# Optimization experiments

Hardware: AMD Instinct MI355X
Metric: run time of the kernel (lower is better)

## Reference

```python
import jax, jax.numpy as jnp
import numpy as np

N_NODES = 50000
N_EDGES = 800000
H = 128
D = 128
N_LAYERS = 4
N_GRAPHS = 128
NODE_VOCAB = 32
EDGE_VOCAB = 8
BN_EPS = 1e-5


def _bn(h, g, b):
    # BatchNorm1d, training-mode statistics (biased variance), as in the torch module
    m = h.mean(axis=0)
    v = ((h - m) ** 2).mean(axis=0)
    return (h - m) * jax.lax.rsqrt(v + BN_EPS) * g + b


def _gine(x, src, dst, e, eps_l):
    # GINEConv: message = ReLU(x_src + edge_attr), sum-aggregate at dst
    msg = jax.nn.relu(x[src] + e)                      # [E, H]
    aggr = jax.ops.segment_sum(msg, dst, num_segments=N_NODES)
    return (1.0 + eps_l) * x + aggr


def _forward(x_ids, edge_index, batch, edge_attr,
             node_emb, edge_emb, eps,
             init_W1, init_b1, init_g1, init_be1, init_W2, init_b2, init_g2, init_be2,
             mp_W1, mp_g1, mp_be1, mp_W2, mp_g2, mp_be2,
             l1_W1, l1_g1, l1_b1, l1_W2, l1_g2, l1_b2,
             l2_W1, l2_g1, l2_b1, l2_W2, l2_g2, l2_b2,
             fin_W):
    src, dst = edge_index[0], edge_index[1]
    x = node_emb[x_ids]                                # [N, H]
    e = edge_emb[edge_attr]                            # [E, H]
    # initialization conv (Linear layers WITH bias)
    h = _gine(x, src, dst, e, eps[0])
    h = jax.nn.relu(_bn(h @ init_W1 + init_b1, init_g1, init_be1))
    x = jax.nn.relu(_bn(h @ init_W2 + init_b2, init_g2, init_be2))
    # message-passing layers (Linear layers WITHOUT bias)
    for i in range(N_LAYERS):
        h = _gine(x, src, dst, e, eps[1 + i])
        h = jax.nn.relu(_bn(h @ mp_W1[i], mp_g1[i], mp_be1[i]))
        x = jax.nn.relu(_bn(h @ mp_W2[i], mp_g2[i], mp_be2[i]))
    # readout: global_add_pool
    g = jax.ops.segment_sum(x, batch, num_segments=N_GRAPHS)   # [G, H]
    # lin1 (outer F.relu is idempotent; dropout = identity in eval)
    h = jax.nn.relu(_bn(g @ l1_W1, l1_g1, l1_b1))
    h = jax.nn.relu(_bn(h @ l1_W2, l1_g2, l1_b2))
    # lin2
    h = jax.nn.relu(_bn(h @ l2_W1, l2_g1, l2_b1))
    h = jax.nn.relu(_bn(h @ l2_W2, l2_g2, l2_b2))
    return h @ fin_W                                   # [G, 1]


def setup_inputs() -> dict:
    key = jax.random.key(0)
    ks = jax.random.split(key, 20)
    s = 1.0 / np.sqrt(H)
    rn = lambda k, shp, sc: jax.random.normal(k, shp, dtype=jnp.float32) * sc
    return {
        "x_ids": jax.random.randint(ks[0], (N_NODES,), 0, NODE_VOCAB),
        "edge_index": jax.random.randint(ks[1], (2, N_EDGES), 0, N_NODES),
        "batch": jnp.sort(jax.random.randint(ks[2], (N_NODES,), 0, N_GRAPHS)),
        "edge_attr": jax.random.randint(ks[14], (N_EDGES,), 0, EDGE_VOCAB),
        "node_emb": rn(ks[3], (NODE_VOCAB, H), 0.05),
        "edge_emb": rn(ks[4], (EDGE_VOCAB, H), 0.05),
        "eps": jnp.zeros((N_LAYERS + 1,), jnp.float32),
        "init_W1": rn(ks[5], (H, D), s), "init_b1": jnp.zeros((D,)),
        "init_g1": jnp.ones((D,)), "init_be1": jnp.zeros((D,)),
        "init_W2": rn(ks[6], (D, H), s), "init_b2": jnp.zeros((H,)),
        "init_g2": jnp.ones((H,)), "init_be2": jnp.zeros((H,)),
        "mp_W1": rn(ks[7], (N_LAYERS, H, D), s),
        "mp_g1": jnp.ones((N_LAYERS, D)), "mp_be1": jnp.zeros((N_LAYERS, D)),
        "mp_W2": rn(ks[8], (N_LAYERS, D, H), s),
        "mp_g2": jnp.ones((N_LAYERS, H)), "mp_be2": jnp.zeros((N_LAYERS, H)),
        "l1_W1": rn(ks[9], (H, D), s), "l1_g1": jnp.ones((D,)), "l1_b1": jnp.zeros((D,)),
        "l1_W2": rn(ks[10], (D, D), s), "l1_g2": jnp.ones((D,)), "l1_b2": jnp.zeros((D,)),
        "l2_W1": rn(ks[11], (D, D), s), "l2_g1": jnp.ones((D,)), "l2_b1": jnp.zeros((D,)),
        "l2_W2": rn(ks[12], (D, H), s), "l2_g2": jnp.ones((H,)), "l2_b2": jnp.zeros((H,)),
        "fin_W": rn(ks[13], (H, 1), s),
    }


def reference(x_ids, edge_index, batch, edge_attr,
              node_emb, edge_emb, eps,
              init_W1, init_b1, init_g1, init_be1, init_W2, init_b2, init_g2, init_be2,
              mp_W1, mp_g1, mp_be1, mp_W2, mp_g2, mp_be2,
              l1_W1, l1_g1, l1_b1, l1_W2, l1_g2, l1_b2,
              l2_W1, l2_g1, l2_b1, l2_W2, l2_g2, l2_b2,
              fin_W):
    return _forward(x_ids, edge_index, batch, edge_attr,
                    node_emb, edge_emb, eps,
                    init_W1, init_b1, init_g1, init_be1, init_W2, init_b2, init_g2, init_be2,
                    mp_W1, mp_g1, mp_be1, mp_W2, mp_g2, mp_be2,
                    l1_W1, l1_g1, l1_b1, l1_W2, l1_g2, l1_b2,
                    l2_W1, l2_g1, l2_b1, l2_W2, l2_g2, l2_b2,
                    fin_W)
```

## Files before the change

kernel.cpp:

```cpp
#include <hip/hip_runtime.h>

#define NN 50000
#define NE 800000
#define NG 128
#define HD 128
#define NL 4
#define BN_EPS 1e-5f
#define REP 32
#define WP 136
#define NB 392
#define EPB 4096

typedef __attribute__((ext_vector_type(8))) short bf16x8;
typedef __attribute__((ext_vector_type(4))) float f32x4;

__device__ __forceinline__ unsigned short f2bf(float f) {
    unsigned u = __float_as_uint(f);
    u += 0x7FFFu + ((u >> 16) & 1u);
    return (unsigned short)(u >> 16);
}
__device__ __forceinline__ float bfval(unsigned short h) { return __uint_as_float((unsigned)h << 16); }
__device__ __forceinline__ float bflo(unsigned u) { return __uint_as_float(u << 16); }
__device__ __forceinline__ float bfhi(unsigned u) { return __uint_as_float(u & 0xFFFF0000u); }

__device__ __forceinline__ void split2(float a, float b, unsigned& hi, unsigned& lo) {
    unsigned ua = __float_as_uint(a), ub = __float_as_uint(b);
    hi = (ua >> 16) | (ub & 0xFFFF0000u);
    float ra = a - __uint_as_float(ua & 0xFFFF0000u);
    float rb = b - __uint_as_float(ub & 0xFFFF0000u);
    lo = (unsigned)f2bf(ra) | ((unsigned)f2bf(rb) << 16);
}
__device__ __forceinline__ unsigned pack2(float a, float b) {
    return (unsigned)f2bf(a) | ((unsigned)f2bf(b) << 16);
}

__device__ __forceinline__ void bn_pre(const float* SQbase,
                                       const float* gam, const float* bet,
                                       float inv_cnt, int t, float* scs, float* shs) {
    if (gam == nullptr) { scs[t] = 1.f; shs[t] = 0.f; return; }
    float s = 0.f, q = 0.f;
#pragma unroll
    for (int r = 0; r < REP; r++) {
        s += SQbase[r * 256 + t];
        q += SQbase[r * 256 + 128 + t];
    }
    float m = s * inv_cnt;
    float var = fmaxf(fmaf(q, inv_cnt, -m * m), 0.f);
    float inv = rsqrtf(var + BN_EPS);
    float sc = gam[t] * inv;
    scs[t] = sc;
    shs[t] = fmaf(-m, sc, bet[t]);
}

__global__ __launch_bounds__(256) void setup_kernel(const int* __restrict__ ids,
                                                    const float* __restrict__ emb,
                                                    unsigned short* __restrict__ Yb,
                                                    const float* __restrict__ iw1,
                                                    const float* __restrict__ iw2,
                                                    const float* __restrict__ mw1,
                                                    const float* __restrict__ mw2,
                                                    const float* __restrict__ hw1,
                                                    const float* __restrict__ hw2,
                                                    const float* __restrict__ hw3,
                                                    const float* __restrict__ hw4,
                                                    unsigned short* __restrict__ Wh,
                                                    unsigned short* __restrict__ Wl,
                                                    const int* __restrict__ dst,
                                                    int* __restrict__ deg) {
    int b = blockIdx.x, t = threadIdx.x;
    if (b < 3125) {
        int i = b * 256 + t;
        if (i < NN * 16) {
            int node = i >> 4, g = i & 15;
            int id = ids[node];
            const float* p = emb + (size_t)id * HD + 8 * g;
            float4 a = *(const float4*)p;
            float4 bb = *(const float4*)(p + 4);
            uint4 o;
            o.x = pack2(a.x, a.y); o.y = pack2(a.z, a.w);
            o.z = pack2(bb.x, bb.y); o.w = pack2(bb.z, bb.w);
            *(uint4*)(Yb + (size_t)node * HD + 8 * g) = o;
        }
    } else if (b < 4021) {
        int i = (b - 3125) * 256 + t;
        if (i < 229376) {
            int seg = i >> 14, loc = i & 16383;
            float v;
            if (seg == 0)       v = iw1[loc];
            else if (seg == 1)  v = iw2[loc];
            else if (seg < 6)   v = mw1[(seg - 2) * 16384 + loc];
            else if (seg < 10)  v = mw2[(seg - 6) * 16384 + loc];
            else if (seg == 10) v = hw1[loc];
            else if (seg == 11) v = hw2[loc];
            else if (seg == 12) v = hw3[loc];
            else                v = hw4[loc];
            int k = loc >> 7, n = loc & 127;
            unsigned short h = f2bf(v);
            float r = v - bfval(h);
            Wh[seg * 16384 + n * 128 + k] = h;
            Wl[seg * 16384 + n * 128 + k] = f2bf(r);
        }
    } else {
        int e = (b - 4021) * 256 + t;
        if (e < NE) atomicAdd(&deg[dst[e]], 1);
    }
}

__global__ __launch_bounds__(256) void ybn_kernel(const float* __restrict__ X,
                                                  const float* __restrict__ SQin,
                                                  const float* __restrict__ gam,
                                                  const float* __restrict__ bet,
                                                  unsigned short* __restrict__ Yb) {
    __shared__ float scs[HD], shs[HD];
    int t = threadIdx.x;
    if (t < HD) bn_pre(SQin, gam, bet, 1.f / NN, t, scs, shs);
    __syncthreads();
    int c8 = (t & 15) * 8;
    float4 s0 = *(const float4*)&scs[c8], s1 = *(const float4*)&scs[c8 + 4];
    float4 h0 = *(const float4*)&shs[c8], h1 = *(const float4*)&shs[c8 + 4];
#pragma unroll
    for (int ch = 0; ch < 4; ch++) {
        int row = blockIdx.x * 64 + ch * 16 + (t >> 4);
        if (row < NN) {
            const float* p = X + (size_t)row * HD + c8;
            float4 v0 = *(const float4*)p;
            float4 v1 = *(const float4*)(p + 4);
            float f0 = fmaxf(fmaf(v0.x, s0.x, h0.x), 0.f), f1 = fmaxf(fmaf(v0.y, s0.y, h0.y), 0.f);
            float f2 = fmaxf(fmaf(v0.z, s0.z, h0.z), 0.f), f3 = fmaxf(fmaf(v0.w, s0.w, h0.w), 0.f);
            float f4 = fmaxf(fmaf(v1.x, s1.x, h1.x), 0.f), f5 = fmaxf(fmaf(v1.y, s1.y, h1.y), 0.f);
            float f6 = fmaxf(fmaf(v1.z, s1.z, h1.z), 0.f), f7 = fmaxf(fmaf(v1.w, s1.w, h1.w), 0.f);
            uint4 o;
            o.x = pack2(f0, f1); o.y = pack2(f2, f3);
            o.z = pack2(f4, f5); o.w = pack2(f6, f7);
            *(uint4*)(Yb + (size_t)row * HD + c8) = o;
        }
    }
}

__global__ __launch_bounds__(1024) void scan1_kernel(const int* __restrict__ deg,
                                                     int* __restrict__ rowptr,
                                                     int* __restrict__ blockSum) {
    __shared__ int s[1024];
    int b = blockIdx.x, t = threadIdx.x;
    int i = b * 1024 + t;
    int v = (i < NN) ? deg[i] : 0;
    s[t] = v;
    __syncthreads();
    for (int off = 1; off < 1024; off <<= 1) {
        int u = (t >= off) ? s[t - off] : 0;
        __syncthreads();
        s[t] += u;
        __syncthreads();
    }
    if (i < NN) rowptr[i] = s[t] - v;
    if (t == 1023) blockSum[b] = s[1023];
}

__global__ __launch_bounds__(64) void scan2_kernel(const int* __restrict__ blockSum,
                                                   int* __restrict__ blockOff,
                                                   int* __restrict__ rowptr, int nblocks) {
    int t = threadIdx.x;
    int orig = (t < nblocks) ? blockSum[t] : 0;
    int v = orig;
    for (int off = 1; off < 64; off <<= 1) {
        int u = __shfl_up(v, off, 64);
        if (t >= off) v += u;
    }
    if (t < nblocks) blockOff[t] = v - orig;
    if (t == nblocks - 1) rowptr[NN] = v;
}

__global__ __launch_bounds__(1024) void scan3_kernel(int* __restrict__ rowptr,
                                                     int* __restrict__ cursor,
                                                     const int* __restrict__ blockOff,
                                                     int* __restrict__ bucketCursor) {
    int b = blockIdx.x, t = threadIdx.x;
    int i = b * 1024 + t;
    if (i < NN) {
        int r = rowptr[i] + blockOff[b];
        rowptr[i] = r;
        cursor[i] = r;
        if ((i & 127) == 0) bucketCursor[i >> 7] = r;
    }
}

__global__ __launch_bounds__(256) void bin_kernel(const int* __restrict__ src,
                                                  const int* __restrict__ dst,
                                                  const int* __restrict__ attr,
                                                  int* __restrict__ bucketCursor,
                                                  uint2* __restrict__ ebuf) {
    __shared__ int cnt[512];
    __shared__ int sc[512], sc2[512];
    __shared__ int base[512];
    __shared__ int garr[NB];
    __shared__ int wof[NB];
    __shared__ uint2 stage[EPB];
    int t = threadIdx.x;
    int e0 = blockIdx.x * EPB;
    for (int i = t; i < 512; i += 256) cnt[i] = 0;
    __syncthreads();
    int myb[16]; unsigned myv[16]; int myd[16];
#pragma unroll
    for (int j = 0; j < 16; j++) {
        int e = e0 + t + j * 256;
        if (e < NE) {
            int d = dst[e];
            myd[j] = d;
            myv[j] = (unsigned)src[e] | ((unsigned)attr[e] << 16);
            myb[j] = d >> 7;
            atomicAdd(&cnt[myb[j]], 1);
        } else myb[j] = -1;
    }
    __syncthreads();
    for (int k = t; k < 512; k += 256) sc[k] = cnt[k];
    __syncthreads();
    int* sp = sc; int* dp = sc2;
    for (int off = 1; off < 512; off <<= 1) {
        for (int k = t; k < 512; k += 256) dp[k] = sp[k] + (k >= off ? sp[k - off] : 0);
        __syncthreads();
        int* tmp = sp; sp = dp; dp = tmp;
    }
    for (int k = t; k < 512; k += 256) base[k] = sp[k] - cnt[k];
    int total = sp[511];
    __syncthreads();
    for (int b = t; b < NB; b += 256) {
        wof[b] = 0;
        if (cnt[b] > 0) garr[b] = atomicAdd(&bucketCursor[b], cnt[b]);
    }
    __syncthreads();
#pragma unroll
    for (int j = 0; j < 16; j++) {
        if (myb[j] >= 0) {
            int slot = base[myb[j]] + atomicAdd(&wof[myb[j]], 1);
            stage[slot] = make_uint2(myv[j], (unsigned)myd[j]);
        }
    }
    __syncthreads();
    for (int i = t; i < total; i += 256) {
        uint2 u = stage[i];
        int b = (int)(u.y >> 7);
        ebuf[garr[b] + (i - base[b])] = u;
    }
}

__global__ __launch_bounds__(256) void place_kernel(const uint2* __restrict__ ebuf,
                                                    const int* __restrict__ rowptr,
                                                    int* __restrict__ cursor,
                                                    unsigned* __restrict__ csr) {
    int b = blockIdx.x;
    int n0 = b * 128;
    int n1 = n0 + 128; if (n1 > NN) n1 = NN;
    int es = rowptr[n0], ee = rowptr[n1];
    for (int i = es + threadIdx.x; i < ee; i += 256) {
        uint2 u = ebuf[i];
        int pos = atomicAdd(&cursor[u.y], 1);
        csr[pos] = u.x;
    }
}

__device__ __forceinline__ void gine_acc(const unsigned short* __restrict__ Yb,
                                         const float* __restrict__ elds,
                                         unsigned p, int cq, float mask, float* a) {
    uint4 q = *(const uint4*)(Yb + (size_t)(p & 0xFFFFu) * HD + 8 * cq);
    const float* ep = elds + (p >> 16) * HD + 8 * cq;
    float4 e0 = *(const float4*)ep;
    float4 e1 = *(const float4*)(ep + 4);
    a[0] += mask * fmaxf(bflo(q.x) + e0.x, 0.f);
    a[1] += mask * fmaxf(bfhi(q.x) + e0.y, 0.f);
    a[2] += mask * fmaxf(bflo(q.y) + e0.z, 0.f);
    a[3] += mask * fmaxf(bfhi(q.y) + e0.w, 0.f);
    a[4] += mask * fmaxf(bflo(q.z) + e1.x, 0.f);
    a[5] += mask * fmaxf(bfhi(q.z) + e1.y, 0.f);
    a[6] += mask * fmaxf(bflo(q.w) + e1.z, 0.f);
    a[7] += mask * fmaxf(bfhi(q.w) + e1.w, 0.f);
}

__global__ __launch_bounds__(256) void conv_kernel(const unsigned short* __restrict__ Yb,
                                                   const int* __restrict__ rowptr,
                                                   const unsigned* __restrict__ csr,
                                                   const float* __restrict__ edge_emb,
                                                   const float* __restrict__ eps, int layer,
                                                   unsigned short* __restrict__ Ah,
                                                   unsigned short* __restrict__ Al) {
    __shared__ float elds[8 * HD];
    int t = threadIdx.x;
    ((float4*)elds)[t] = ((const float4*)edge_emb)[t];
    __syncthreads();
    int wave = t >> 6, lane = t & 63;
    int node = blockIdx.x * 4 + wave;
    if (node >= NN) return;
    int sub = lane >> 4, cq = lane & 15;
    int lo = rowptr[node], hi = rowptr[node + 1];
    float a[8];
#pragma unroll
    for (int i = 0; i < 8; i++) a[i] = 0.f;
    for (int base = lo; base < hi; base += 64) {
        unsigned pl = 0;
        int cnt = hi - base; if (cnt > 64) cnt = 64;
        if (base + lane < hi) pl = csr[base + lane];
        int j = 0;
        for (; j + 16 <= cnt; j += 16) {
            unsigned pa = __shfl(pl, j + sub, 64);
            unsigned pb = __shfl(pl, j + 4 + sub, 64);
            unsigned pc = __shfl(pl, j + 8 + sub, 64);
            unsigned pd = __shfl(pl, j + 12 + sub, 64);
            gine_acc(Yb, elds, pa, cq, 1.f, a);
            gine_acc(Yb, elds, pb, cq, 1.f, a);
            gine_acc(Yb, elds, pc, cq, 1.f, a);
            gine_acc(Yb, elds, pd, cq, 1.f, a);
        }
        for (; j + 8 <= cnt; j += 8) {
            unsigned pa = __shfl(pl, j + sub, 64);
            unsigned pb = __shfl(pl, j + 4 + sub, 64);
            gine_acc(Yb, elds, pa, cq, 1.f, a);
            gine_acc(Yb, elds, pb, cq, 1.f, a);
        }
        for (; j < cnt; j += 4) {
            int je = j + sub;
            bool val = (je < cnt);
            unsigned p = __shfl(pl, val ? je : j, 64);
            gine_acc(Yb, elds, p, cq, val ? 1.f : 0.f, a);
        }
    }
#pragma unroll
    for (int i = 0; i < 8; i++) {
        a[i] += __shfl_xor(a[i], 16, 64);
        a[i] += __shfl_xor(a[i], 32, 64);
    }
    if (sub == 0) {
        float g = 1.f + eps[layer];
        uint4 q = *(const uint4*)(Yb + (size_t)node * HD + 8 * cq);
        float o0 = fmaf(g, bflo(q.x), a[0]), o1 = fmaf(g, bfhi(q.x), a[1]);
        float o2 = fmaf(g, bflo(q.y), a[2]), o3 = fmaf(g, bfhi(q.y), a[3]);
        float o4 = fmaf(g, bflo(q.z), a[4]), o5 = fmaf(g, bfhi(q.z), a[5]);
        float o6 = fmaf(g, bflo(q.w), a[6]), o7 = fmaf(g, bfhi(q.w), a[7]);
        uint4 H, L;
        split2(o0, o1, H.x, L.x);
        split2(o2, o3, H.y, L.y);
        split2(o4, o5, H.z, L.z);
        split2(o6, o7, H.w, L.w);
        *(uint4*)(Ah + (size_t)node * HD + 8 * cq) = H;
        *(uint4*)(Al + (size_t)node * HD + 8 * cq) = L;
    }
}

__global__ __launch_bounds__(512) void mm_mfma_pre(const unsigned short* __restrict__ Ah,
                                                   const unsigned short* __restrict__ Al,
                                                   const unsigned short* __restrict__ Wh,
                                                   const unsigned short* __restrict__ Wl,
                                                   const float* __restrict__ bias,
                                                   float* __restrict__ out,
                                                   float* __restrict__ SQout) {
    __shared__ unsigned short WhS[128 * WP];
    __shared__ unsigned short WlS[128 * WP];
    int t = threadIdx.x;
    int rowblk = blockIdx.x;
#pragma unroll
    for (int i = 0; i < 4; i++) {
        int idx = t + i * 512;
        int col = idx >> 4, kk = (idx & 15) * 8;
        *(uint4*)(WhS + col * WP + kk) = *(const uint4*)(Wh + (size_t)col * HD + kk);
        *(uint4*)(WlS + col * WP + kk) = *(const uint4*)(Wl + (size_t)col * HD + kk);
    }
    __syncthreads();
    int w = t >> 6, lane = t & 63;
    int quad = lane >> 4, nl = lane & 15;
    int row0 = rowblk * 128 + w * 16;
    int rA0 = row0 + nl;
    bool ok0 = rA0 < NN;
    f32x4 acc[8];
#pragma unroll
    for (int i = 0; i < 8; i++) acc[i] = (f32x4){0.f, 0.f, 0.f, 0.f};
#pragma unroll
    for (int kc = 0; kc < 4; kc++) {
        int k0 = kc * 32 + quad * 8;
        bf16x8 a0h = ok0 ? *(const bf16x8*)(Ah + (size_t)rA0 * HD + k0) : (bf16x8)0;
        bf16x8 a0l = ok0 ? *(const bf16x8*)(Al + (size_t)rA0 * HD + k0) : (bf16x8)0;
#pragma unroll
        for (int c = 0; c < 8; c++) {
            int wof = (c * 16 + nl) * WP + k0;
            bf16x8 bh = *(const bf16x8*)(WhS + wof);
            bf16x8 bl = *(const bf16x8*)(WlS + wof);
            acc[c] = __builtin_amdgcn_mfma_f32_16x16x32_bf16(a0h, bh, acc[c], 0, 0, 0);
            acc[c] = __builtin_amdgcn_mfma_f32_16x16x32_bf16(a0l, bh, acc[c], 0, 0, 0);
            acc[c] = __builtin_amdgcn_mfma_f32_16x16x32_bf16(a0h, bl, acc[c], 0, 0, 0);
        }
    }
    int rep = (blockIdx.x & (REP - 1)) * 256;
    int baserow = row0 + quad * 4;
#pragma unroll
    for (int c = 0; c < 8; c++) {
        int col = c * 16 + nl;
        float bv = bias ? bias[col] : 0.f;
        f32x4 v = acc[c];
        float s = 0.f, qq = 0.f;
#pragma unroll
        for (int r = 0; r < 4; r++) {
            int grow = baserow + r;
            float val = v[r] + bv;
            if (grow < NN) {
                out[(size_t)grow * HD + col] = val;
                s += val;
                qq += val * val;
            }
        }
        s += __shfl_xor(s, 16, 64);  s += __shfl_xor(s, 32, 64);
        qq += __shfl_xor(qq, 16, 64); qq += __shfl_xor(qq, 32, 64);
        if (quad == 0) {
            atomicAdd(&SQout[rep + col], s);
            atomicAdd(&SQout[rep + 128 + col], qq);
        }
    }
}

__global__ __launch_bounds__(512) void mm_mfma_act(const float* __restrict__ A,
                                                   const unsigned short* __restrict__ Wh,
                                                   const unsigned short* __restrict__ Wl,
                                                   const float* __restrict__ bias,
                                                   const float* __restrict__ SQin,
                                                   const float* __restrict__ gam,
                                                   const float* __restrict__ bet,
                                                   float* __restrict__ out,
                                                   float* __restrict__ SQout) {
    __shared__ unsigned short WhS[128 * WP];
    __shared__ unsigned short WlS[128 * WP];
    __shared__ float scs[HD], shs[HD];
    int t = threadIdx.x;
    int rowblk = blockIdx.x;
    if (t < HD) bn_pre(SQin, gam, bet, 1.f / NN, t, scs, shs);
#pragma unroll
    for (int i = 0; i < 4; i++) {
        int idx = t + i * 512;
        int col = idx >> 4, kk = (idx & 15) * 8;
        *(uint4*)(WhS + col * WP + kk) = *(const uint4*)(Wh + (size_t)col * HD + kk);
        *(uint4*)(WlS + col * WP + kk) = *(const uint4*)(Wl + (size_t)col * HD + kk);
    }
    __syncthreads();
    int w = t >> 6, lane = t & 63;
    int quad = lane >> 4, nl = lane & 15;
    int row0 = rowblk * 128 + w * 16;
    int rA0 = row0 + nl;
    bool ok0 = rA0 < NN;
    f32x4 acc[8];
#pragma unroll
    for (int i = 0; i < 8; i++) acc[i] = (f32x4){0.f, 0.f, 0.f, 0.f};
#pragma unroll
    for (int kc = 0; kc < 4; kc++) {
        int k0 = kc * 32 + quad * 8;
        float4 s0 = *(const float4*)&scs[k0], s1 = *(const float4*)&scs[k0 + 4];
        float4 t0 = *(const float4*)&shs[k0], t1 = *(const float4*)&shs[k0 + 4];
        bf16x8 a0h, a0l;
        {
            float4 v0 = ok0 ? *(const float4*)(A + (size_t)rA0 * HD + k0) : make_float4(0, 0, 0, 0);
            float4 v1 = ok0 ? *(const float4*)(A + (size_t)rA0 * HD + k0 + 4) : make_float4(0, 0, 0, 0);
            float f0 = fmaxf(fmaf(v0.x, s0.x, t0.x), 0.f), f1 = fmaxf(fmaf(v0.y, s0.y, t0.y), 0.f);
            float f2 = fmaxf(fmaf(v0.z, s0.z, t0.z), 0.f), f3 = fmaxf(fmaf(v0.w, s0.w, t0.w), 0.f);
            float f4 = fmaxf(fmaf(v1.x, s1.x, t1.x), 0.f), f5 = fmaxf(fmaf(v1.y, s1.y, t1.y), 0.f);
            float f6 = fmaxf(fmaf(v1.z, s1.z, t1.z), 0.f), f7 = fmaxf(fmaf(v1.w, s1.w, t1.w), 0.f);
            if (!ok0) { f0 = f1 = f2 = f3 = f4 = f5 = f6 = f7 = 0.f; }
            unsigned h0, h1, h2, h3, l0, l1, l2, l3;
            split2(f0, f1, h0, l0); split2(f2, f3, h1, l1);
            split2(f4, f5, h2, l2); split2(f6, f7, h3, l3);
            a0h = __builtin_bit_cast(bf16x8, make_uint4(h0, h1, h2, h3));
            a0l = __builtin_bit_cast(bf16x8, make_uint4(l0, l1, l2, l3));
        }
#pragma unroll
        for (int c = 0; c < 8; c++) {
            int wof = (c * 16 + nl) * WP + k0;
            bf16x8 bh = *(const bf16x8*)(WhS + wof);
            bf16x8 bl = *(const bf16x8*)(WlS + wof);
            acc[c] = __builtin_amdgcn_mfma_f32_16x16x32_bf16(a0h, bh, acc[c], 0, 0, 0);
            acc[c] = __builtin_amdgcn_mfma_f32_16x16x32_bf16(a0l, bh, acc[c], 0, 0, 0);
            acc[c] = __builtin_amdgcn_mfma_f32_16x16x32_bf16(a0h, bl, acc[c], 0, 0, 0);
        }
    }
    int rep = (blockIdx.x & (REP - 1)) * 256;
    int baserow = row0 + quad * 4;
#pragma unroll
    for (int c = 0; c < 8; c++) {
        int col = c * 16 + nl;
        float bv = bias ? bias[col] : 0.f;
        f32x4 v = acc[c];
        float s = 0.f, qq = 0.f;
#pragma unroll
        for (int r = 0; r < 4; r++) {
            int grow = baserow + r;
            float val = v[r] + bv;
            if (grow < NN) {
                out[(size_t)grow * HD + col] = val;
                s += val;
                qq += val * val;
            }
        }
        s += __shfl_xor(s, 16, 64);  s += __shfl_xor(s, 32, 64);
        qq += __shfl_xor(qq, 16, 64); qq += __shfl_xor(qq, 32, 64);
        if (quad == 0) {
            atomicAdd(&SQout[rep + col], s);
            atomicAdd(&SQout[rep + 128 + col], qq);
        }
    }
}

__global__ __launch_bounds__(256) void readout_kernel(const float* __restrict__ x,
                                                      const int* __restrict__ batch,
                                                      const float* __restrict__ SQin,
                                                      const float* __restrict__ gam,
                                                      const float* __restrict__ bet,
                                                      float* __restrict__ gout) {
    __shared__ int bat[256];
    __shared__ float scs[HD], shs[HD];
    int t = threadIdx.x;
    int rq = t >> 5, cq = t & 31;
    int r0 = blockIdx.x * 256;
    int i = r0 + t;
    bat[t] = (i < NN) ? batch[i] : -1;
    if (t < HD) bn_pre(SQin, gam, bet, 1.f / NN, t, scs, shs);
    __syncthreads();
    float4 s4 = *(const float4*)&scs[4 * cq];
    float4 h4 = *(const float4*)&shs[4 * cq];
    float4 acc = make_float4(0.f, 0.f, 0.f, 0.f);
    int gcur = -1;
    for (int j = rq; j < 256; j += 8) {
        int r = r0 + j;
        if (r >= NN) break;
        int g = bat[j];
        if (g != gcur) {
            if (gcur >= 0) {
                atomicAdd(&gout[(size_t)gcur * HD + 4 * cq + 0], acc.x);
                atomicAdd(&gout[(size_t)gcur * HD + 4 * cq + 1], acc.y);
                atomicAdd(&gout[(size_t)gcur * HD + 4 * cq + 2], acc.z);
                atomicAdd(&gout[(size_t)gcur * HD + 4 * cq + 3], acc.w);
            }
            acc = make_float4(0.f, 0.f, 0.f, 0.f);
            gcur = g;
        }
        float4 v = *(const float4*)(x + (size_t)r * HD + 4 * cq);
        acc.x += fmaxf(fmaf(v.x, s4.x, h4.x), 0.f);
        acc.y += fmaxf(fmaf(v.y, s4.y, h4.y), 0.f);
        acc.z += fmaxf(fmaf(v.z, s4.z, h4.z), 0.f);
        acc.w += fmaxf(fmaf(v.w, s4.w, h4.w), 0.f);
    }
    if (gcur >= 0) {
        atomicAdd(&gout[(size_t)gcur * HD + 4 * cq + 0], acc.x);
        atomicAdd(&gout[(size_t)gcur * HD + 4 * cq + 1], acc.y);
        atomicAdd(&gout[(size_t)gcur * HD + 4 * cq + 2], acc.z);
        atomicAdd(&gout[(size_t)gcur * HD + 4 * cq + 3], acc.w);
    }
}

__device__ __forceinline__ void head_stage(const unsigned short* __restrict__ Whg,
                                           const unsigned short* __restrict__ Wlg,
                                           const float* __restrict__ gam,
                                           const float* __restrict__ bet,
                                           float* A_lds,
                                           unsigned short* WhS, unsigned short* WlS,
                                           float* colS, float* colQ,
                                           float* scs, float* shs) {
    const int AP = 132;
    int t = threadIdx.x;
#pragma unroll
    for (int i = 0; i < 2; i++) {
        int idx = t + i * 1024;
        int col = idx >> 4, kk = (idx & 15) * 8;
        *(uint4*)(WhS + col * WP + kk) = *(const uint4*)(Whg + (size_t)col * HD + kk);
        *(uint4*)(WlS + col * WP + kk) = *(const uint4*)(Wlg + (size_t)col * HD + kk);
    }
    __syncthreads();
    int w = t >> 6, lane = t & 63;
    int quad = lane >> 4, nl = lane & 15;
    int row0 = (w >> 2) * 32, col0 = (w & 3) * 32;
    f32x4 acc[4];
#pragma unroll
    for (int i = 0; i < 4; i++) acc[i] = (f32x4){0.f, 0.f, 0.f, 0.f};
#pragma unroll
    for (int kc = 0; kc < 4; kc++) {
        int k0 = kc * 32 + quad * 8;
        float4 s0 = *(const float4*)&scs[k0], s1 = *(const float4*)&scs[k0 + 4];
        float4 t0 = *(const float4*)&shs[k0], t1 = *(const float4*)&shs[k0 + 4];
        bf16x8 a0h, a0l, a1h, a1l;
        {
            const float* ap = &A_lds[(row0 + nl) * AP + k0];
            float4 v0 = *(const float4*)ap;
            float4 v1 = *(const float4*)(ap + 4);
            float f0 = fmaxf(fmaf(v0.x, s0.x, t0.x), 0.f), f1 = fmaxf(fmaf(v0.y, s0.y, t0.y), 0.f);
            float f2 = fmaxf(fmaf(v0.z, s0.z, t0.z), 0.f), f3 = fmaxf(fmaf(v0.w, s0.w, t0.w), 0.f);
            float f4 = fmaxf(fmaf(v1.x, s1.x, t1.x), 0.f), f5 = fmaxf(fmaf(v1.y, s1.y, t1.y), 0.f);
            float f6 = fmaxf(fmaf(v1.z, s1.z, t1.z), 0.f), f7 = fmaxf(fmaf(v1.w, s1.w, t1.w), 0.f);
            unsigned h0, h1, h2, h3, l0, l1, l2, l3;
            split2(f0, f1, h0, l0); split2(f2, f3, h1, l1);
            split2(f4, f5, h2, l2); split2(f6, f7, h3, l3);
            a0h = __builtin_bit_cast(bf16x8, make_uint4(h0, h1, h2, h3));
            a0l = __builtin_bit_cast(bf16x8, make_uint4(l0, l1, l2, l3));
        }
        {
            const float* ap = &A_lds[(row0 + 16 + nl) * AP + k0];
            float4 v0 = *(const float4*)ap;
            float4 v1 = *(const float4*)(ap + 4);
            float f0 = fmaxf(fmaf(v0.x, s0.x, t0.x), 0.f), f1 = fmaxf(fmaf(v0.y, s0.y, t0.y), 0.f);
            float f2 = fmaxf(fmaf(v0.z, s0.z, t0.z), 0.f), f3 = fmaxf(fmaf(v0.w, s0.w, t0.w), 0.f);
            float f4 = fmaxf(fmaf(v1.x, s1.x, t1.x), 0.f), f5 = fmaxf(fmaf(v1.y, s1.y, t1.y), 0.f);
            float f6 = fmaxf(fmaf(v1.z, s1.z, t1.z), 0.f), f7 = fmaxf(fmaf(v1.w, s1.w, t1.w), 0.f);
            unsigned h0, h1, h2, h3, l0, l1, l2, l3;
            split2(f0, f1, h0, l0); split2(f2, f3, h1, l1);
            split2(f4, f5, h2, l2); split2(f6, f7, h3, l3);
            a1h = __builtin_bit_cast(bf16x8, make_uint4(h0, h1, h2, h3));
            a1l = __builtin_bit_cast(bf16x8, make_uint4(l0, l1, l2, l3));
        }
#pragma unroll
        for (int cc = 0; cc < 2; cc++) {
            int wof = (col0 + cc * 16 + nl) * WP + k0;
            bf16x8 bh = *(const bf16x8*)(WhS + wof);
            bf16x8 bl = *(const bf16x8*)(WlS + wof);
            acc[cc] = __builtin_amdgcn_mfma_f32_16x16x32_bf16(a0h, bh, acc[cc], 0, 0, 0);
            acc[cc] = __builtin_amdgcn_mfma_f32_16x16x32_bf16(a0l, bh, acc[cc], 0, 0, 0);
            acc[cc] = __builtin_amdgcn_mfma_f32_16x16x32_bf16(a0h, bl, acc[cc], 0, 0, 0);
            acc[2 + cc] = __builtin_amdgcn_mfma_f32_16x16x32_bf16(a1h, bh, acc[2 + cc], 0, 0, 0);
            acc[2 + cc] = __builtin_amdgcn_mfma_f32_16x16x32_bf16(a1l, bh, acc[2 + cc], 0, 0, 0);
            acc[2 + cc] = __builtin_amdgcn_mfma_f32_16x16x32_bf16(a1h, bl, acc[2 + cc], 0, 0, 0);
        }
    }
    __syncthreads();
#pragma unroll
    for (int h = 0; h < 2; h++) {
        int baserow = row0 + h * 16 + quad * 4;
#pragma unroll
        for (int cc = 0; cc < 2; cc++) {
            int col = col0 + cc * 16 + nl;
            f32x4 v = acc[h * 2 + cc];
            float ss = 0.f, qq = 0.f;
#pragma unroll
            for (int r = 0; r < 4; r++) {
                float val = v[r];
                A_lds[(baserow + r) * AP + col] = val;
                ss += val;
                qq += val * val;
            }
            ss += __shfl_xor(ss, 16, 64);  ss += __shfl_xor(ss, 32, 64);
            qq += __shfl_xor(qq, 16, 64);  qq += __shfl_xor(qq, 32, 64);
            if (quad == 0) {
                atomicAdd(&colS[col], ss);
                atomicAdd(&colQ[col], qq);
            }
        }
    }
    __syncthreads();
    if (t < HD) {
        float m = colS[t] * (1.f / NG);
        float var = fmaxf(fmaf(colQ[t], 1.f / NG, -m * m), 0.f);
        float inv = rsqrtf(var + BN_EPS);
        float sc = gam[t] * inv;
        scs[t] = sc;
        shs[t] = fmaf(-m, sc, bet[t]);
        colS[t] = 0.f;
        colQ[t] = 0.f;
    }
    __syncthreads();
}

__global__ __launch_bounds__(1024) void head_fused(const float* __restrict__ Gp,
                                                   const unsigned short* __restrict__ Whd,
                                                   const unsigned short* __restrict__ Wld,
                                                   const float* __restrict__ g0,
                                                   const float* __restrict__ b0,
                                                   const float* __restrict__ g1,
                                                   const float* __restrict__ b1,
                                                   const float* __restrict__ g2,
                                                   const float* __restrict__ b2,
                                                   const float* __restrict__ g3,
                                                   const float* __restrict__ b3,
                                                   const float* __restrict__ finW,
                                                   float* __restrict__ out) {
    const int AP = 132;
    __shared__ float A_lds[128 * AP];
    __shared__ unsigned short WhS[128 * WP];
    __shared__ unsigned short WlS[128 * WP];
    __shared__ float colS[HD], colQ[HD], scs[HD], shs[HD];
    int t = threadIdx.x;
    if (t < HD) { colS[t] = 0.f; colQ[t] = 0.f; scs[t] = 1.f; shs[t] = 0.f; }
#pragma unroll
    for (int i = 0; i < 4; i++) {
        int idx = t + i * 1024;
        int r = idx >> 5, cq = (idx & 31) * 4;
        *(float4*)&A_lds[r * AP + cq] = *(const float4*)(Gp + (size_t)r * HD + cq);
    }
    head_stage(Whd + 0 * 16384, Wld + 0 * 16384, g0, b0, A_lds, WhS, WlS, colS, colQ, scs, shs);
    head_stage(Whd + 1 * 16384, Wld + 1 * 16384, g1, b1, A_lds, WhS, WlS, colS, colQ, scs, shs);
    head_stage(Whd + 2 * 16384, Wld + 2 * 16384, g2, b2, A_lds, WhS, WlS, colS, colQ, scs, shs);
    head_stage(Whd + 3 * 16384, Wld + 3 * 16384, g3, b3, A_lds, WhS, WlS, colS, colQ, scs, shs);
    int r = t >> 3, g = t & 7;
    float ssum = 0.f;
#pragma unroll
    for (int j = 0; j < 16; j++) {
        int c = g * 16 + j;
        float v = fmaxf(fmaf(A_lds[r * AP + c], scs[c], shs[c]), 0.f);
        ssum += v * finW[c];
    }
    ssum += __shfl_xor(ssum, 1, 64);
    ssum += __shfl_xor(ssum, 2, 64);
    ssum += __shfl_xor(ssum, 4, 64);
    if (g == 0) out[r] = ssum;
}

extern "C" void kernel_launch(void* const* d_in, const int* in_sizes, int n_in,
                              void* d_out, int out_size, void* d_ws, size_t ws_size,
                              hipStream_t stream) {
    const int* x_ids = (const int*)d_in[0];
    const int* edge_index = (const int*)d_in[1];
    const int* batch = (const int*)d_in[2];
    const int* edge_attr = (const int*)d_in[3];
    const float* node_emb = (const float*)d_in[4];
    const float* edge_emb = (const float*)d_in[5];
    const float* eps = (const float*)d_in[6];
    const float* init_W1 = (const float*)d_in[7];
    const float* init_b1 = (const float*)d_in[8];
    const float* init_g1 = (const float*)d_in[9];
    const float* init_be1 = (const float*)d_in[10];
    const float* init_W2 = (const float*)d_in[11];
    const float* init_b2 = (const float*)d_in[12];
    const float* init_g2 = (const float*)d_in[13];
    const float* init_be2 = (const float*)d_in[14];
    const float* mp_W1 = (const float*)d_in[15];
    const float* mp_g1 = (const float*)d_in[16];
    const float* mp_be1 = (const float*)d_in[17];
    const float* mp_W2 = (const float*)d_in[18];
    const float* mp_g2 = (const float*)d_in[19];
    const float* mp_be2 = (const float*)d_in[20];
    const float* l1_W1 = (const float*)d_in[21];
    const float* l1_g1 = (const float*)d_in[22];
    const float* l1_b1 = (const float*)d_in[23];
    const float* l1_W2 = (const float*)d_in[24];
    const float* l1_g2 = (const float*)d_in[25];
    const float* l1_b2 = (const float*)d_in[26];
    const float* l2_W1 = (const float*)d_in[27];
    const float* l2_g1 = (const float*)d_in[28];
    const float* l2_b1 = (const float*)d_in[29];
    const float* l2_W2 = (const float*)d_in[30];
    const float* l2_g2 = (const float*)d_in[31];
    const float* l2_b2 = (const float*)d_in[32];
    const float* fin_W = (const float*)d_in[33];

    const int* e_src = edge_index;
    const int* e_dst = edge_index + NE;

    const size_t STG = (size_t)REP * 256;
    float* ws = (float*)d_ws;
    float* X = ws;
    float* Bbuf = X + (size_t)NN * HD;
    unsigned short* Yb = (unsigned short*)Bbuf;
    unsigned short* Ah = (unsigned short*)(Bbuf + (size_t)NN * HD);
    unsigned short* Al = Ah + (size_t)NN * HD;
    float* SQ = (float*)(Al + (size_t)NN * HD);
    float* Gp = SQ + 14 * STG;
    int* deg = (int*)(Gp + NG * HD);
    float* Hp = (float*)(deg + 50048);
    float* Hp2 = Hp + NG * HD;
    int* rowptr = (int*)(Hp2 + NG * HD);
    int* cursor = rowptr + 50048;
    int* blockSum = cursor + 50048;
    int* blockOff = blockSum + 64;
    int* bucketCursor = blockOff + 64;
    unsigned* csr = (unsigned*)(bucketCursor + NB);
    unsigned short* Wh = (unsigned short*)(csr + NE);
    unsigned short* Wl = Wh + 229376;
    uint2* ebuf = (uint2*)(Wl + 229376);
    (void)Hp; (void)Hp2;

    const size_t zero_bytes = (14 * STG + NG * HD) * sizeof(float) + 50048 * sizeof(int);
    hipMemsetAsync(SQ, 0, zero_bytes, stream);

    const int SCAN_BLOCKS = (NN + 1023) / 1024;
    setup_kernel<<<7146, 256, 0, stream>>>(x_ids, node_emb, Yb, init_W1, init_W2, mp_W1,
                                           mp_W2, l1_W1, l1_W2, l2_W1, l2_W2,
                                           Wh, Wl, e_dst, deg);
    scan1_kernel<<<SCAN_BLOCKS, 1024, 0, stream>>>(deg, rowptr, blockSum);
    scan2_kernel<<<1, 64, 0, stream>>>(blockSum, blockOff, rowptr, SCAN_BLOCKS);
    scan3_kernel<<<SCAN_BLOCKS, 1024, 0, stream>>>(rowptr, cursor, blockOff, bucketCursor);
    bin_kernel<<<(NE + EPB - 1) / EPB, 256, 0, stream>>>(e_src, e_dst, edge_attr,
                                                         bucketCursor, ebuf);
    place_kernel<<<(NN + 127) / 128, 256, 0, stream>>>(ebuf, rowptr, cursor, csr);

    const int mfma_grid = (NN + 127) / 128;
    const int ybn_grid = (NN + 63) / 64;
    for (int i = 0; i <= NL; i++) {
        const unsigned short* Wh1 = Wh + (size_t)(i == 0 ? 0 : 2 + (i - 1)) * 16384;
        const unsigned short* Wl1 = Wl + (size_t)(i == 0 ? 0 : 2 + (i - 1)) * 16384;
        const unsigned short* Wh2 = Wh + (size_t)(i == 0 ? 1 : 6 + (i - 1)) * 16384;
        const unsigned short* Wl2 = Wl + (size_t)(i == 0 ? 1 : 6 + (i - 1)) * 16384;
        const float* b1 = (i == 0) ? init_b1 : nullptr;
        const float* b2 = (i == 0) ? init_b2 : nullptr;
        const float* g1 = (i == 0) ? init_g1 : mp_g1 + (size_t)(i - 1) * HD;
        const float* be1 = (i == 0) ? init_be1 : mp_be1 + (size_t)(i - 1) * HD;
        const float* gp = (i == 1) ? init_g2 : mp_g2 + (size_t)(i - 2) * HD;
        const float* bp = (i == 1) ? init_be2 : mp_be2 + (size_t)(i - 2) * HD;
        float* Sprev = SQ + (size_t)(2 * i - 1) * STG;
        float* S1 = SQ + (size_t)(2 * i) * STG;
        float* S2 = SQ + (size_t)(2 * i + 1) * STG;

        if (i > 0) ybn_kernel<<<ybn_grid, 256, 0, stream>>>(X, Sprev, gp, bp, Yb);
        conv_kernel<<<(NN + 3) / 4, 256, 0, stream>>>(Yb, rowptr, csr, edge_emb, eps, i, Ah, Al);
        mm_mfma_pre<<<mfma_grid, 512, 0, stream>>>(Ah, Al, Wh1, Wl1, b1, Bbuf, S1);
        mm_mfma_act<<<mfma_grid, 512, 0, stream>>>(Bbuf, Wh2, Wl2, b2, S1, g1, be1, X, S2);
    }

    float* S9 = SQ + 9 * STG;
    readout_kernel<<<(NN + 255) / 256, 256, 0, stream>>>(
        X, batch, S9, mp_g2 + 3 * HD, mp_be2 + 3 * HD, Gp);

    head_fused<<<1, 1024, 0, stream>>>(Gp, Wh + (size_t)10 * 16384, Wl + (size_t)10 * 16384,
                                       l1_g1, l1_b1, l1_g2, l1_b2,
                                       l2_g1, l2_b1, l2_g2, l2_b2,
                                       fin_W, (float*)d_out);
}
```

Baseline: 686.0 us.

## Fold scan2 into scan3, specialize full-tile epilogues, prefetch head weights

Removes the single-wave scan2 launch by having every scan3 block recompute the 64-entry block-offset prefix in its first wave, saving one kernel launch in the setup chain. The matmul epilogues get a branch-free path for full 128-row tiles, dropping per-row bounds checks. The head kernel inlines its four stages and prefetches the next stage's weights into registers while the current stage computes. The cost is redundant prefix work in each scan3 block and some code growth from the duplicated epilogue.

```diff
diff --git a/kernel.cpp b/kernel.cpp
--- a/kernel.cpp
+++ b/kernel.cpp
@@ -156,32 +156,32 @@
     if (t == 1023) blockSum[b] = s[1023];
 }
 
-__global__ __launch_bounds__(64) void scan2_kernel(const int* __restrict__ blockSum,
-                                                   int* __restrict__ blockOff,
-                                                   int* __restrict__ rowptr, int nblocks) {
-    int t = threadIdx.x;
-    int orig = (t < nblocks) ? blockSum[t] : 0;
-    int v = orig;
-    for (int off = 1; off < 64; off <<= 1) {
-        int u = __shfl_up(v, off, 64);
-        if (t >= off) v += u;
-    }
-    if (t < nblocks) blockOff[t] = v - orig;
-    if (t == nblocks - 1) rowptr[NN] = v;
-}
-
 __global__ __launch_bounds__(1024) void scan3_kernel(int* __restrict__ rowptr,
                                                      int* __restrict__ cursor,
-                                                     const int* __restrict__ blockOff,
-                                                     int* __restrict__ bucketCursor) {
+                                                     const int* __restrict__ blockSum,
+                                                     int* __restrict__ bucketCursor,
+                                                     int nblocks) {
+    __shared__ int sOff, sTot;
     int b = blockIdx.x, t = threadIdx.x;
+    if (t < 64) {
+        int orig = (t < nblocks) ? blockSum[t] : 0;
+        int v = orig;
+        for (int off = 1; off < 64; off <<= 1) {
+            int u = __shfl_up(v, off, 64);
+            if (t >= off) v += u;
+        }
+        if (t == b) sOff = v - orig;
+        if (t == nblocks - 1) sTot = v;
+    }
+    __syncthreads();
     int i = b * 1024 + t;
     if (i < NN) {
-        int r = rowptr[i] + blockOff[b];
+        int r = rowptr[i] + sOff;
         rowptr[i] = r;
         cursor[i] = r;
         if ((i & 127) == 0) bucketCursor[i >> 7] = r;
     }
+    if (b == nblocks - 1 && t == 0) rowptr[NN] = sTot;
 }
 
 __global__ __launch_bounds__(256) void bin_kernel(const int* __restrict__ src,
@@ -388,27 +388,50 @@
     }
     int rep = (blockIdx.x & (REP - 1)) * 256;
     int baserow = row0 + quad * 4;
-#pragma unroll
-    for (int c = 0; c < 8; c++) {
-        int col = c * 16 + nl;
-        float bv = bias ? bias[col] : 0.f;
-        f32x4 v = acc[c];
-        float s = 0.f, qq = 0.f;
-#pragma unroll
-        for (int r = 0; r < 4; r++) {
-            int grow = baserow + r;
-            float val = v[r] + bv;
-            if (grow < NN) {
-                out[(size_t)grow * HD + col] = val;
+    if (rowblk * 128 + 128 <= NN) {
+#pragma unroll
+        for (int c = 0; c < 8; c++) {
+            int col = c * 16 + nl;
+            float bv = bias ? bias[col] : 0.f;
+            f32x4 v = acc[c];
+            float s = 0.f, qq = 0.f;
+#pragma unroll
+            for (int r = 0; r < 4; r++) {
+                float val = v[r] + bv;
+                out[(size_t)(baserow + r) * HD + col] = val;
                 s += val;
                 qq += val * val;
             }
-        }
-        s += __shfl_xor(s, 16, 64);  s += __shfl_xor(s, 32, 64);
-        qq += __shfl_xor(qq, 16, 64); qq += __shfl_xor(qq, 32, 64);
-        if (quad == 0) {
-            atomicAdd(&SQout[rep + col], s);
-            atomicAdd(&SQout[rep + 128 + col], qq);
+            s += __shfl_xor(s, 16, 64);  s += __shfl_xor(s, 32, 64);
+            qq += __shfl_xor(qq, 16, 64); qq += __shfl_xor(qq, 32, 64);
+            if (quad == 0) {
+                atomicAdd(&SQout[rep + col], s);
+                atomicAdd(&SQout[rep + 128 + col], qq);
+            }
+        }
+    } else {
+#pragma unroll
+        for (int c = 0; c < 8; c++) {
+            int col = c * 16 + nl;
+            float bv = bias ? bias[col] : 0.f;
+            f32x4 v = acc[c];
+            float s = 0.f, qq = 0.f;
+#pragma unroll
+            for (int r = 0; r < 4; r++) {
+                int grow = baserow + r;
+                float val = v[r] + bv;
+                if (grow < NN) {
+                    out[(size_t)grow * HD + col] = val;
+                    s += val;
+                    qq += val * val;
+                }
+            }
+            s += __shfl_xor(s, 16, 64);  s += __shfl_xor(s, 32, 64);
+            qq += __shfl_xor(qq, 16, 64); qq += __shfl_xor(qq, 32, 64);
+            if (quad == 0) {
+                atomicAdd(&SQout[rep + col], s);
+                atomicAdd(&SQout[rep + 128 + col], qq);
+            }
         }
     }
 }
@@ -476,27 +499,50 @@
     }
     int rep = (blockIdx.x & (REP - 1)) * 256;
     int baserow = row0 + quad * 4;
-#pragma unroll
-    for (int c = 0; c < 8; c++) {
-        int col = c * 16 + nl;
-        float bv = bias ? bias[col] : 0.f;
-        f32x4 v = acc[c];
-        float s = 0.f, qq = 0.f;
-#pragma unroll
-        for (int r = 0; r < 4; r++) {
-            int grow = baserow + r;
-            float val = v[r] + bv;
-            if (grow < NN) {
-                out[(size_t)grow * HD + col] = val;
+    if (rowblk * 128 + 128 <= NN) {
+#pragma unroll
+        for (int c = 0; c < 8; c++) {
+            int col = c * 16 + nl;
+            float bv = bias ? bias[col] : 0.f;
+            f32x4 v = acc[c];
+            float s = 0.f, qq = 0.f;
+#pragma unroll
+            for (int r = 0; r < 4; r++) {
+                float val = v[r] + bv;
+                out[(size_t)(baserow + r) * HD + col] = val;
                 s += val;
                 qq += val * val;
             }
-        }
-        s += __shfl_xor(s, 16, 64);  s += __shfl_xor(s, 32, 64);
-        qq += __shfl_xor(qq, 16, 64); qq += __shfl_xor(qq, 32, 64);
-        if (quad == 0) {
-            atomicAdd(&SQout[rep + col], s);
-            atomicAdd(&SQout[rep + 128 + col], qq);
+            s += __shfl_xor(s, 16, 64);  s += __shfl_xor(s, 32, 64);
+            qq += __shfl_xor(qq, 16, 64); qq += __shfl_xor(qq, 32, 64);
+            if (quad == 0) {
+                atomicAdd(&SQout[rep + col], s);
+                atomicAdd(&SQout[rep + 128 + col], qq);
+            }
+        }
+    } else {
+#pragma unroll
+        for (int c = 0; c < 8; c++) {
+            int col = c * 16 + nl;
+            float bv = bias ? bias[col] : 0.f;
+            f32x4 v = acc[c];
+            float s = 0.f, qq = 0.f;
+#pragma unroll
+            for (int r = 0; r < 4; r++) {
+                int grow = baserow + r;
+                float val = v[r] + bv;
+                if (grow < NN) {
+                    out[(size_t)grow * HD + col] = val;
+                    s += val;
+                    qq += val * val;
+                }
+            }
+            s += __shfl_xor(s, 16, 64);  s += __shfl_xor(s, 32, 64);
+            qq += __shfl_xor(qq, 16, 64); qq += __shfl_xor(qq, 32, 64);
+            if (quad == 0) {
+                atomicAdd(&SQout[rep + col], s);
+                atomicAdd(&SQout[rep + 128 + col], qq);
+            }
         }
     }
 }
@@ -546,115 +592,6 @@
         atomicAdd(&gout[(size_t)gcur * HD + 4 * cq + 2], acc.z);
         atomicAdd(&gout[(size_t)gcur * HD + 4 * cq + 3], acc.w);
     }
-}
-
-__device__ __forceinline__ void head_stage(const unsigned short* __restrict__ Whg,
-                                           const unsigned short* __restrict__ Wlg,
-                                           const float* __restrict__ gam,
-                                           const float* __restrict__ bet,
-                                           float* A_lds,
-                                           unsigned short* WhS, unsigned short* WlS,
-                                           float* colS, float* colQ,
-                                           float* scs, float* shs) {
-    const int AP = 132;
-    int t = threadIdx.x;
-#pragma unroll
-    for (int i = 0; i < 2; i++) {
-        int idx = t + i * 1024;
-        int col = idx >> 4, kk = (idx & 15) * 8;
-        *(uint4*)(WhS + col * WP + kk) = *(const uint4*)(Whg + (size_t)col * HD + kk);
-        *(uint4*)(WlS + col * WP + kk) = *(const uint4*)(Wlg + (size_t)col * HD + kk);
-    }
-    __syncthreads();
-    int w = t >> 6, lane = t & 63;
-    int quad = lane >> 4, nl = lane & 15;
-    int row0 = (w >> 2) * 32, col0 = (w & 3) * 32;
-    f32x4 acc[4];
-#pragma unroll
-    for (int i = 0; i < 4; i++) acc[i] = (f32x4){0.f, 0.f, 0.f, 0.f};
-#pragma unroll
-    for (int kc = 0; kc < 4; kc++) {
-        int k0 = kc * 32 + quad * 8;
-        float4 s0 = *(const float4*)&scs[k0], s1 = *(const float4*)&scs[k0 + 4];
-        float4 t0 = *(const float4*)&shs[k0], t1 = *(const float4*)&shs[k0 + 4];
-        bf16x8 a0h, a0l, a1h, a1l;
-        {
-            const float* ap = &A_lds[(row0 + nl) * AP + k0];
-            float4 v0 = *(const float4*)ap;
-            float4 v1 = *(const float4*)(ap + 4);
-            float f0 = fmaxf(fmaf(v0.x, s0.x, t0.x), 0.f), f1 = fmaxf(fmaf(v0.y, s0.y, t0.y), 0.f);
-            float f2 = fmaxf(fmaf(v0.z, s0.z, t0.z), 0.f), f3 = fmaxf(fmaf(v0.w, s0.w, t0.w), 0.f);
-            float f4 = fmaxf(fmaf(v1.x, s1.x, t1.x), 0.f), f5 = fmaxf(fmaf(v1.y, s1.y, t1.y), 0.f);
-            float f6 = fmaxf(fmaf(v1.z, s1.z, t1.z), 0.f), f7 = fmaxf(fmaf(v1.w, s1.w, t1.w), 0.f);
-            unsigned h0, h1, h2, h3, l0, l1, l2, l3;
-            split2(f0, f1, h0, l0); split2(f2, f3, h1, l1);
-            split2(f4, f5, h2, l2); split2(f6, f7, h3, l3);
-            a0h = __builtin_bit_cast(bf16x8, make_uint4(h0, h1, h2, h3));
-            a0l = __builtin_bit_cast(bf16x8, make_uint4(l0, l1, l2, l3));
-        }
-        {
-            const float* ap = &A_lds[(row0 + 16 + nl) * AP + k0];
-            float4 v0 = *(const float4*)ap;
-            float4 v1 = *(const float4*)(ap + 4);
-            float f0 = fmaxf(fmaf(v0.x, s0.x, t0.x), 0.f), f1 = fmaxf(fmaf(v0.y, s0.y, t0.y), 0.f);
-            float f2 = fmaxf(fmaf(v0.z, s0.z, t0.z), 0.f), f3 = fmaxf(fmaf(v0.w, s0.w, t0.w), 0.f);
-            float f4 = fmaxf(fmaf(v1.x, s1.x, t1.x), 0.f), f5 = fmaxf(fmaf(v1.y, s1.y, t1.y), 0.f);
-            float f6 = fmaxf(fmaf(v1.z, s1.z, t1.z), 0.f), f7 = fmaxf(fmaf(v1.w, s1.w, t1.w), 0.f);
-            unsigned h0, h1, h2, h3, l0, l1, l2, l3;
-            split2(f0, f1, h0, l0); split2(f2, f3, h1, l1);
-            split2(f4, f5, h2, l2); split2(f6, f7, h3, l3);
-            a1h = __builtin_bit_cast(bf16x8, make_uint4(h0, h1, h2, h3));
-            a1l = __builtin_bit_cast(bf16x8, make_uint4(l0, l1, l2, l3));
-        }
-#pragma unroll
-        for (int cc = 0; cc < 2; cc++) {
-            int wof = (col0 + cc * 16 + nl) * WP + k0;
-            bf16x8 bh = *(const bf16x8*)(WhS + wof);
-            bf16x8 bl = *(const bf16x8*)(WlS + wof);
-            acc[cc] = __builtin_amdgcn_mfma_f32_16x16x32_bf16(a0h, bh, acc[cc], 0, 0, 0);
-            acc[cc] = __builtin_amdgcn_mfma_f32_16x16x32_bf16(a0l, bh, acc[cc], 0, 0, 0);
-            acc[cc] = __builtin_amdgcn_mfma_f32_16x16x32_bf16(a0h, bl, acc[cc], 0, 0, 0);
-            acc[2 + cc] = __builtin_amdgcn_mfma_f32_16x16x32_bf16(a1h, bh, acc[2 + cc], 0, 0, 0);
-            acc[2 + cc] = __builtin_amdgcn_mfma_f32_16x16x32_bf16(a1l, bh, acc[2 + cc], 0, 0, 0);
-            acc[2 + cc] = __builtin_amdgcn_mfma_f32_16x16x32_bf16(a1h, bl, acc[2 + cc], 0, 0, 0);
-        }
-    }
-    __syncthreads();
-#pragma unroll
-    for (int h = 0; h < 2; h++) {
-        int baserow = row0 + h * 16 + quad * 4;
-#pragma unroll
-        for (int cc = 0; cc < 2; cc++) {
-            int col = col0 + cc * 16 + nl;
-            f32x4 v = acc[h * 2 + cc];
-            float ss = 0.f, qq = 0.f;
-#pragma unroll
-            for (int r = 0; r < 4; r++) {
-                float val = v[r];
-                A_lds[(baserow + r) * AP + col] = val;
-                ss += val;
-                qq += val * val;
-            }
-            ss += __shfl_xor(ss, 16, 64);  ss += __shfl_xor(ss, 32, 64);
-            qq += __shfl_xor(qq, 16, 64);  qq += __shfl_xor(qq, 32, 64);
-            if (quad == 0) {
-                atomicAdd(&colS[col], ss);
-                atomicAdd(&colQ[col], qq);
-            }
-        }
-    }
-    __syncthreads();
-    if (t < HD) {
-        float m = colS[t] * (1.f / NG);
-        float var = fmaxf(fmaf(colQ[t], 1.f / NG, -m * m), 0.f);
-        float inv = rsqrtf(var + BN_EPS);
-        float sc = gam[t] * inv;
-        scs[t] = sc;
-        shs[t] = fmaf(-m, sc, bet[t]);
-        colS[t] = 0.f;
-        colQ[t] = 0.f;
-    }
-    __syncthreads();
 }
 
 __global__ __launch_bounds__(1024) void head_fused(const float* __restrict__ Gp,
@@ -683,10 +620,119 @@
         int r = idx >> 5, cq = (idx & 31) * 4;
         *(float4*)&A_lds[r * AP + cq] = *(const float4*)(Gp + (size_t)r * HD + cq);
     }
-    head_stage(Whd + 0 * 16384, Wld + 0 * 16384, g0, b0, A_lds, WhS, WlS, colS, colQ, scs, shs);
-    head_stage(Whd + 1 * 16384, Wld + 1 * 16384, g1, b1, A_lds, WhS, WlS, colS, colQ, scs, shs);
-    head_stage(Whd + 2 * 16384, Wld + 2 * 16384, g2, b2, A_lds, WhS, WlS, colS, colQ, scs, shs);
-    head_stage(Whd + 3 * 16384, Wld + 3 * 16384, g3, b3, A_lds, WhS, WlS, colS, colQ, scs, shs);
+    int sc_ = t >> 4;
+    int sk_ = (t & 15) * 8;
+    const float* gs[4] = {g0, g1, g2, g3};
+    const float* bs[4] = {b0, b1, b2, b3};
+    uint4 ph0 = *(const uint4*)(Whd + (size_t)sc_ * HD + sk_);
+    uint4 ph1 = *(const uint4*)(Whd + (size_t)(sc_ + 64) * HD + sk_);
+    uint4 pl0 = *(const uint4*)(Wld + (size_t)sc_ * HD + sk_);
+    uint4 pl1 = *(const uint4*)(Wld + (size_t)(sc_ + 64) * HD + sk_);
+    int w = t >> 6, lane = t & 63;
+    int quad = lane >> 4, nl = lane & 15;
+    int row0 = (w >> 2) * 32, col0 = (w & 3) * 32;
+#pragma unroll
+    for (int s = 0; s < 4; s++) {
+        *(uint4*)(WhS + sc_ * WP + sk_) = ph0;
+        *(uint4*)(WhS + (sc_ + 64) * WP + sk_) = ph1;
+        *(uint4*)(WlS + sc_ * WP + sk_) = pl0;
+        *(uint4*)(WlS + (sc_ + 64) * WP + sk_) = pl1;
+        __syncthreads();
+        if (s < 3) {
+            const unsigned short* nh = Whd + (size_t)(s + 1) * 16384;
+            const unsigned short* nl2 = Wld + (size_t)(s + 1) * 16384;
+            ph0 = *(const uint4*)(nh + (size_t)sc_ * HD + sk_);
+            ph1 = *(const uint4*)(nh + (size_t)(sc_ + 64) * HD + sk_);
+            pl0 = *(const uint4*)(nl2 + (size_t)sc_ * HD + sk_);
+            pl1 = *(const uint4*)(nl2 + (size_t)(sc_ + 64) * HD + sk_);
+        }
+        f32x4 acc[4];
+#pragma unroll
+        for (int i = 0; i < 4; i++) acc[i] = (f32x4){0.f, 0.f, 0.f, 0.f};
+#pragma unroll
+        for (int kc = 0; kc < 4; kc++) {
+            int k0 = kc * 32 + quad * 8;
+            float4 s0 = *(const float4*)&scs[k0], s1 = *(const float4*)&scs[k0 + 4];
+            float4 t0 = *(const float4*)&shs[k0], t1 = *(const float4*)&shs[k0 + 4];
+            bf16x8 a0h, a0l, a1h, a1l;
+            {
+                const float* ap = &A_lds[(row0 + nl) * AP + k0];
+                float4 v0 = *(const float4*)ap;
+                float4 v1 = *(const float4*)(ap + 4);
+                float f0 = fmaxf(fmaf(v0.x, s0.x, t0.x), 0.f), f1 = fmaxf(fmaf(v0.y, s0.y, t0.y), 0.f);
+                float f2 = fmaxf(fmaf(v0.z, s0.z, t0.z), 0.f), f3 = fmaxf(fmaf(v0.w, s0.w, t0.w), 0.f);
+                float f4 = fmaxf(fmaf(v1.x, s1.x, t1.x), 0.f), f5 = fmaxf(fmaf(v1.y, s1.y, t1.y), 0.f);
+                float f6 = fmaxf(fmaf(v1.z, s1.z, t1.z), 0.f), f7 = fmaxf(fmaf(v1.w, s1.w, t1.w), 0.f);
+                unsigned h0, h1, h2, h3, l0, l1, l2, l3;
+                split2(f0, f1, h0, l0); split2(f2, f3, h1, l1);
+                split2(f4, f5, h2, l2); split2(f6, f7, h3, l3);
+                a0h = __builtin_bit_cast(bf16x8, make_uint4(h0, h1, h2, h3));
+                a0l = __builtin_bit_cast(bf16x8, make_uint4(l0, l1, l2, l3));
+            }
+            {
+                const float* ap = &A_lds[(row0 + 16 + nl) * AP + k0];
+                float4 v0 = *(const float4*)ap;
+                float4 v1 = *(const float4*)(ap + 4);
+                float f0 = fmaxf(fmaf(v0.x, s0.x, t0.x), 0.f), f1 = fmaxf(fmaf(v0.y, s0.y, t0.y), 0.f);
+                float f2 = fmaxf(fmaf(v0.z, s0.z, t0.z), 0.f), f3 = fmaxf(fmaf(v0.w, s0.w, t0.w), 0.f);
+                float f4 = fmaxf(fmaf(v1.x, s1.x, t1.x), 0.f), f5 = fmaxf(fmaf(v1.y, s1.y, t1.y), 0.f);
+                float f6 = fmaxf(fmaf(v1.z, s1.z, t1.z), 0.f), f7 = fmaxf(fmaf(v1.w, s1.w, t1.w), 0.f);
+                unsigned h0, h1, h2, h3, l0, l1, l2, l3;
+                split2(f0, f1, h0, l0); split2(f2, f3, h1, l1);
+                split2(f4, f5, h2, l2); split2(f6, f7, h3, l3);
+                a1h = __builtin_bit_cast(bf16x8, make_uint4(h0, h1, h2, h3));
+                a1l = __builtin_bit_cast(bf16x8, make_uint4(l0, l1, l2, l3));
+            }
+#pragma unroll
+            for (int cc = 0; cc < 2; cc++) {
+                int wof = (col0 + cc * 16 + nl) * WP + k0;
+                bf16x8 bh = *(const bf16x8*)(WhS + wof);
+                bf16x8 bl = *(const bf16x8*)(WlS + wof);
+                acc[cc] = __builtin_amdgcn_mfma_f32_16x16x32_bf16(a0h, bh, acc[cc], 0, 0, 0);
+                acc[cc] = __builtin_amdgcn_mfma_f32_16x16x32_bf16(a0l, bh, acc[cc], 0, 0, 0);
+                acc[cc] = __builtin_amdgcn_mfma_f32_16x16x32_bf16(a0h, bl, acc[cc], 0, 0, 0);
+                acc[2 + cc] = __builtin_amdgcn_mfma_f32_16x16x32_bf16(a1h, bh, acc[2 + cc], 0, 0, 0);
+                acc[2 + cc] = __builtin_amdgcn_mfma_f32_16x16x32_bf16(a1l, bh, acc[2 + cc], 0, 0, 0);
+                acc[2 + cc] = __builtin_amdgcn_mfma_f32_16x16x32_bf16(a1h, bl, acc[2 + cc], 0, 0, 0);
+            }
+        }
+        __syncthreads();
+#pragma unroll
+        for (int h = 0; h < 2; h++) {
+            int baserow = row0 + h * 16 + quad * 4;
+#pragma unroll
+            for (int cc = 0; cc < 2; cc++) {
+                int col = col0 + cc * 16 + nl;
+                f32x4 v = acc[h * 2 + cc];
+                float ss = 0.f, qq = 0.f;
+#pragma unroll
+                for (int r = 0; r < 4; r++) {
+                    float val = v[r];
+                    A_lds[(baserow + r) * AP + col] = val;
+                    ss += val;
+                    qq += val * val;
+                }
+                ss += __shfl_xor(ss, 16, 64);  ss += __shfl_xor(ss, 32, 64);
+                qq += __shfl_xor(qq, 16, 64);  qq += __shfl_xor(qq, 32, 64);
+                if (quad == 0) {
+                    atomicAdd(&colS[col], ss);
+                    atomicAdd(&colQ[col], qq);
+                }
+            }
+        }
+        __syncthreads();
+        if (t < HD) {
+            float m = colS[t] * (1.f / NG);
+            float var = fmaxf(fmaf(colQ[t], 1.f / NG, -m * m), 0.f);
+            float inv = rsqrtf(var + BN_EPS);
+            float sc = gs[s][t] * inv;
+            scs[t] = sc;
+            shs[t] = fmaf(-m, sc, bs[s][t]);
+            colS[t] = 0.f;
+            colQ[t] = 0.f;
+        }
+        __syncthreads();
+    }
     int r = t >> 3, g = t & 7;
     float ssum = 0.f;
 #pragma unroll
@@ -763,7 +809,7 @@
     unsigned short* Wh = (unsigned short*)(csr + NE);
     unsigned short* Wl = Wh + 229376;
     uint2* ebuf = (uint2*)(Wl + 229376);
-    (void)Hp; (void)Hp2;
+    (void)Hp; (void)Hp2; (void)blockOff;
 
     const size_t zero_bytes = (14 * STG + NG * HD) * sizeof(float) + 50048 * sizeof(int);
     hipMemsetAsync(SQ, 0, zero_bytes, stream);
@@ -773,8 +819,8 @@
                                            mp_W2, l1_W1, l1_W2, l2_W1, l2_W2,
                                            Wh, Wl, e_dst, deg);
     scan1_kernel<<<SCAN_BLOCKS, 1024, 0, stream>>>(deg, rowptr, blockSum);
-    scan2_kernel<<<1, 64, 0, stream>>>(blockSum, blockOff, rowptr, SCAN_BLOCKS);
-    scan3_kernel<<<SCAN_BLOCKS, 1024, 0, stream>>>(rowptr, cursor, blockOff, bucketCursor);
+    scan3_kernel<<<SCAN_BLOCKS, 1024, 0, stream>>>(rowptr, cursor, blockSum, bucketCursor,
+                                                   SCAN_BLOCKS);
     bin_kernel<<<(NE + EPB - 1) / EPB, 256, 0, stream>>>(e_src, e_dst, edge_attr,
                                                          bucketCursor, ebuf);
     place_kernel<<<(NN + 127) / 128, 256, 0, stream>>>(ebuf, rowptr, cursor, csr);
```

Result: no change. 675.7 us (-1.5%).
